# Performance work log

Hardware: AMD Instinct MI355X
Metric: run time of the kernel (lower is better)

## Reference

```python
import jax, jax.numpy as jnp
import numpy as np

NBINS = (128, 64, 32)
N_REGIONS = 5000
N_REGIONS_OI = 500
N_POINTS = 262144
SUM_H = sum(NBINS)            # 224
SUM_W = sum(n - 1 for n in NBINS)  # 221


def _spline_level(x, uw_region, uh_pt, local_ix):
    """One quadratic-spline level.
    x: [N] inputs in [0,1); uw_region: [R, n-1] region unnormalized widths;
    uh_pt: [N, n] per-point unnormalized heights (embedding + delta);
    local_ix: [N] int mapping points -> rows of uw_region.
    """
    # region-level widths / bin locations (calculate_widths / calculate_bin_locations)
    widths = jax.nn.softmax(uw_region, axis=-1)                # [R, n-1]
    bl = jnp.cumsum(widths, axis=-1)
    bl = bl.at[:, -1].set(1.0)
    bin_locations = jnp.pad(bl, ((0, 0), (1, 0)))              # [R, n]

    # gather per point (index_select(0, local_region_ix))
    widths_pt = widths[local_ix]                               # [N, n-1]
    bin_loc_pt = bin_locations[local_ix]                       # [N, n]

    # calculate_heights: exp then normalize so trapezoid integral == 1
    he = jnp.exp(uh_pt)                                        # [N, n]
    area = jnp.sum(0.5 * (he[:, :-1] + he[:, 1:]) * widths_pt, axis=-1, keepdims=True)
    heights = he / area                                        # [N, n]

    # calculate_bin_left_cdf
    cdf = jnp.cumsum(0.5 * (heights[:, :-1] + heights[:, 1:]) * widths_pt, axis=-1)
    cdf = cdf.at[:, -1].set(1.0)
    bin_left_cdf = jnp.pad(cdf, ((0, 0), (1, 0)))              # [N, n]

    # searchsorted(bin_locations, x, side='left') - 1, clamped to valid bins
    n = bin_loc_pt.shape[-1]
    bin_idx = jnp.clip(jnp.sum(bin_loc_pt < x[:, None], axis=-1) - 1, 0, n - 2)  # [N]

    take = lambda a, i: jnp.take_along_axis(a, i[:, None], axis=-1)[:, 0]
    in_loc = take(bin_loc_pt, bin_idx)
    in_w = take(widths_pt, bin_idx)
    in_cdf = take(bin_left_cdf, bin_idx)
    h_l = take(heights, bin_idx)
    h_r = take(heights, bin_idx + 1)

    alpha = (x - in_loc) / in_w
    a = 0.5 * (h_r - h_l) * in_w
    b = h_l * in_w
    out = a * alpha * alpha + b * alpha + in_cdf
    logabsdet = jnp.log(alpha * (h_r - h_l) + h_l)
    return out, logabsdet


def setup_inputs() -> dict:
    key = jax.random.key(0)
    k1, k2, k3, k4, k5, k6 = jax.random.split(key, 6)
    x = jax.random.uniform(k1, (N_POINTS,), dtype=jnp.float32)
    regions_oi = jax.random.randint(k2, (N_REGIONS_OI,), 0, N_REGIONS, dtype=jnp.int32)
    local_region_ix = jax.random.randint(k3, (N_POINTS,), 0, N_REGIONS_OI, dtype=jnp.int32)
    delta = jax.random.normal(k4, (N_POINTS, SUM_H), dtype=jnp.float32)
    # learned sparse embedding tables (init to random for a nontrivial baseline)
    heights_emb = 0.1 * jax.random.normal(k5, (N_REGIONS, SUM_H), dtype=jnp.float32)
    widths_emb = 0.1 * jax.random.normal(k6, (N_REGIONS, SUM_W), dtype=jnp.float32)
    return {"x": x, "regions_oi": regions_oi, "local_region_ix": local_region_ix,
            "delta": delta, "heights_emb": heights_emb, "widths_emb": widths_emb}


def reference(x, regions_oi, local_region_ix, delta, heights_emb, widths_emb):
    uh_all = heights_emb[regions_oi]   # [R, 224]
    uw_all = widths_emb[regions_oi]    # [R, 221]
    out = x
    logdet = jnp.zeros_like(x)
    oh = 0
    ow = 0
    for n in NBINS:
        uw = uw_all[:, ow:ow + (n - 1)]                               # [R, n-1]
        uh_pt = uh_all[local_region_ix][:, oh:oh + n] + delta[:, oh:oh + n]  # [N, n]
        out, ld = _spline_level(out, uw, uh_pt, local_region_ix)
        logdet = logdet + ld
        oh += n
        ow += n - 1
    return out, logdet
```

## Files before the change

### kernel.cpp

```cpp
#include <hip/hip_runtime.h>

#define NPOINTS 262144
#define SUMH 224
#define SUMW 221
#define NREG 500

__device__ __forceinline__ float rlane(float v, int l) {
  return __int_as_float(__builtin_amdgcn_readlane(__float_as_int(v), l));
}
template<int CTRL>
__device__ __forceinline__ float dpp0(float x) {
  return __int_as_float(__builtin_amdgcn_update_dpp(0, __float_as_int(x), CTRL, 0xF, 0xF, true));
}
template<int CTRL, int RM>
__device__ __forceinline__ float dpp_rm(float x) {
  return __int_as_float(__builtin_amdgcn_update_dpp(0, __float_as_int(x), CTRL, RM, 0xF, false));
}
template<int CTRL>
__device__ __forceinline__ float dpp_max_(float x) {
  return fmaxf(x, __int_as_float(__builtin_amdgcn_update_dpp(__float_as_int(x), __float_as_int(x), CTRL, 0xF, 0xF, false)));
}
__device__ __forceinline__ float wave_sum(float x) {
  x += dpp0<0x111>(x); x += dpp0<0x112>(x); x += dpp0<0x114>(x); x += dpp0<0x118>(x);
  x += dpp_rm<0x142, 0xA>(x); x += dpp_rm<0x143, 0xC>(x);
  return rlane(x, 63);
}
__device__ __forceinline__ float wave_max(float x) {
  x = dpp_max_<0x111>(x); x = dpp_max_<0x112>(x); x = dpp_max_<0x114>(x);
  x = dpp_max_<0x118>(x); x = dpp_max_<0x142>(x); x = dpp_max_<0x143>(x);
  return rlane(x, 63);
}
__device__ __forceinline__ float wave_scan_incl(float x) {
  x += dpp0<0x111>(x); x += dpp0<0x112>(x); x += dpp0<0x114>(x); x += dpp0<0x118>(x);
  x += dpp_rm<0x142, 0xA>(x);
  x += dpp_rm<0x143, 0xC>(x);
  return x;
}
__device__ __forceinline__ float grp_sum(float x) {
  x += dpp0<0xB1>(x);
  x += dpp0<0x4E>(x);
  x += dpp0<0x141>(x);
  x += dpp0<0x140>(x);
  return x;
}


template<int M, int SRC, int DST, int NB>
__device__ __forceinline__ void region_level(const float* __restrict__ wrow,
    float* __restrict__ BL, float* __restrict__ HW, float* __restrict__ HS,
    int lane, float* lds)
{
  float v0 = (lane < M) ? wrow[SRC + lane] : -1e30f;
  float v1 = -1e30f;
  if constexpr (NB == 128) { if (lane + 64 < M) v1 = wrow[SRC + lane + 64]; }
  float m = wave_max(fmaxf(v0, v1));
  float e0 = __expf(v0 - m);
  float e1 = (NB == 128) ? __expf(v1 - m) : 0.0f;
  float s = wave_sum(e0 + e1);
  float inv = 1.0f / s;
  if (lane < NB) lds[lane] = e0;
  if constexpr (NB == 128) lds[lane + 64] = e1;
  __syncthreads();
  if (lane < NB) {
    HW[DST + lane] = 0.5f * e0 * inv;
    float prev = (lane == 0) ? 0.0f : lds[lane - 1];
    HS[DST + lane] = 0.5f * (e0 + prev) * inv;
  }
  if constexpr (NB == 128) {
    HW[DST + lane + 64] = 0.5f * e1 * inv;
    HS[DST + lane + 64] = 0.5f * (e1 + lds[lane + 63]) * inv;
  }
  float incl0 = wave_scan_incl(e0);
  if (lane == 0) BL[DST] = 0.0f;
  if (lane < M) BL[DST + 1 + lane] = (lane == M - 1) ? 1.0f : incl0 * inv;
  if constexpr (NB == 128) {
    float incl1 = wave_scan_incl(e1) + rlane(incl0, 63);
    int k = 64 + lane;
    if (k < M) BL[DST + 1 + k] = (k == M - 1) ? 1.0f : incl1 * inv;
  }
  __syncthreads();
}

__global__ void __launch_bounds__(64) region_kernel(
    const int* __restrict__ roi, const float* __restrict__ wemb,
    float* __restrict__ wsBL, float* __restrict__ wsHW, float* __restrict__ wsHS)
{
  __shared__ float lds[128];
  int rix = blockIdx.x;
  int lane = threadIdx.x;
  int greg = roi[rix];
  const float* wrow = wemb + (size_t)greg * SUMW;
  float* BL = wsBL + (size_t)rix * SUMH;
  float* HW = wsHW + (size_t)rix * SUMH;
  float* HS = wsHS + (size_t)rix * SUMH;
  region_level<127,   0,   0, 128>(wrow, BL, HW, HS, lane, lds);
  region_level< 63, 127, 128,  64>(wrow, BL, HW, HS, lane, lds);
  region_level< 31, 190, 192,  32>(wrow, BL, HW, HS, lane, lds);
}


template<int NB, int OFF, int C>
struct Lv {
  float he[C], t[C], bl[C], hw[C];
  float larea, invarea;

  __device__ __forceinline__ void prep(const float* __restrict__ U,
      const float* __restrict__ D, const float* __restrict__ BLt,
      const float* __restrict__ HWt, const float* __restrict__ HSt, int s)
  {
    if constexpr (C >= 4) {
#pragma unroll
      for (int v = 0; v < C / 4; ++v) {
        int c0 = OFF + (s * (C / 4) + v) * 4;
        float4 a = *(const float4*)(U   + c0);
        float4 b = *(const float4*)(D   + c0);
        float4 e = *(const float4*)(BLt + c0);
        float4 f = *(const float4*)(HWt + c0);
        float4 g = *(const float4*)(HSt + c0);
        he[4*v+0] = __expf(a.x + b.x); he[4*v+1] = __expf(a.y + b.y);
        he[4*v+2] = __expf(a.z + b.z); he[4*v+3] = __expf(a.w + b.w);
        t[4*v+0] = he[4*v+0] * g.x; t[4*v+1] = he[4*v+1] * g.y;
        t[4*v+2] = he[4*v+2] * g.z; t[4*v+3] = he[4*v+3] * g.w;
        bl[4*v+0]=e.x; bl[4*v+1]=e.y; bl[4*v+2]=e.z; bl[4*v+3]=e.w;
        hw[4*v+0]=f.x; hw[4*v+1]=f.y; hw[4*v+2]=f.z; hw[4*v+3]=f.w;
      }
    } else {
      int c0 = OFF + s * 2;
      float2 a = *(const float2*)(U   + c0);
      float2 b = *(const float2*)(D   + c0);
      float2 e = *(const float2*)(BLt + c0);
      float2 f = *(const float2*)(HWt + c0);
      float2 g = *(const float2*)(HSt + c0);
      he[0] = __expf(a.x + b.x); he[1] = __expf(a.y + b.y);
      t[0] = he[0] * g.x; t[1] = he[1] * g.y;
      bl[0]=e.x; bl[1]=e.y; hw[0]=f.x; hw[1]=f.y;
    }
    float asum = 0.0f;
#pragma unroll
    for (int i = 0; i < C; ++i) asum += t[i];
    float area = grp_sum(asum);
    larea = __log2f(area);
    invarea = __builtin_amdgcn_rcpf(area);
  }

  __device__ __forceinline__ void apply(float& xv, float& logdet, int s) {
    float f[C];
#pragma unroll
    for (int i = 0; i < C; ++i) f[i] = (bl[i] < xv) ? 1.0f : 0.0f;
    if (s == 0)  f[0]     = 1.0f;
    if (s == 15) f[C - 1] = 0.0f;
    float fN  = dpp0<0x101>(f[0]);
    float heN = dpp0<0x101>(he[0]);
    float hl = 0.0f, hr = 0.0f, loc = 0.0f, hwm = 0.0f, pt = 0.0f;
#pragma unroll
    for (int i = 0; i < C; ++i) {
      float fnext  = (i < C - 1) ? f[i + 1]  : fN;
      float henext = (i < C - 1) ? he[i + 1] : heN;
      float mi = f[i] * (1.0f - fnext);
      hl  += he[i] * mi;
      hr  += henext * mi;
      loc += bl[i] * mi;
      hwm += hw[i] * mi;
      pt  += t[i] * f[i];
    }
    hl  = grp_sum(hl);
    hr  = grp_sum(hr);
    loc = grp_sum(loc);
    hwm = grp_sum(hwm);
    pt  = grp_sum(pt);
    float part = pt - hl * hwm;
    float inw = 2.0f * hwm;
    float alpha = (xv - loc) * __builtin_amdgcn_rcpf(inw);
    float dh = hr - hl;
    xv = ((0.5f * dh * alpha + hl) * alpha * inw + part) * invarea;
    logdet += (__log2f(alpha * dh + hl) - larea) * 0.69314718055994531f;
  }
};

__global__ void __launch_bounds__(256) spline_kernel(
    const float* __restrict__ x, const int* __restrict__ roi,
    const int* __restrict__ lix, const float* __restrict__ delta,
    const float* __restrict__ hemb,
    const float* __restrict__ wsBL, const float* __restrict__ wsHW,
    const float* __restrict__ wsHS, float* __restrict__ out)
{
  int tid  = (int)(blockIdx.x * blockDim.x + threadIdx.x);
  int wid  = tid >> 6;
  int lane = (int)(threadIdx.x & 63);
  int grp  = lane >> 4;
  int s    = lane & 15;
  int pid  = wid * 4 + grp;

  float xv = x[pid];
  int r    = lix[pid];
  int greg = roi[r];
  const float* U   = hemb  + (size_t)greg * SUMH;
  const float* D   = delta + (size_t)pid  * SUMH;
  const float* BLt = wsBL  + (size_t)r    * SUMH;
  const float* HWt = wsHW  + (size_t)r    * SUMH;
  const float* HSt = wsHS  + (size_t)r    * SUMH;

  Lv<128,   0, 8> L0;
  Lv< 64, 128, 4> L1;
  Lv< 32, 192, 2> L2;
  float logdet = 0.0f;
  L0.prep(U, D, BLt, HWt, HSt, s);
  L1.prep(U, D, BLt, HWt, HSt, s);
  L0.apply(xv, logdet, s);
  L2.prep(U, D, BLt, HWt, HSt, s);
  L1.apply(xv, logdet, s);
  L2.apply(xv, logdet, s);

  if (s == 0) {
    out[pid] = xv;
    out[NPOINTS + pid] = logdet;
  }
}


extern "C" void kernel_launch(void* const* d_in, const int* in_sizes, int n_in,
                              void* d_out, int out_size, void* d_ws, size_t ws_size,
                              hipStream_t stream) {
  const float* x     = (const float*)d_in[0];
  const int*   roi   = (const int*)  d_in[1];
  const int*   lix   = (const int*)  d_in[2];
  const float* delta = (const float*)d_in[3];
  const float* hemb  = (const float*)d_in[4];
  const float* wemb  = (const float*)d_in[5];

  float* wsBL = (float*)d_ws;
  float* wsHW = wsBL + (size_t)NREG * SUMH;
  float* wsHS = wsHW + (size_t)NREG * SUMH;

  region_kernel<<<NREG, 64, 0, stream>>>(roi, wemb, wsBL, wsHW, wsHS);
  spline_kernel<<<NPOINTS / 16, 256, 0, stream>>>(x, roi, lix, delta, hemb,
                                                  wsBL, wsHW, wsHS, (float*)d_out);
}
```

Before: 358.7 us.

## Map each point to 32 lanes instead of 16 in spline kernel

Each point is now processed by a half-wave of 32 lanes rather than 16, so each lane holds fewer bins per level (4/2/1 instead of 8/4/2). Group reductions gain a ds_swizzle step, and the neighbour exchange moves from DPP row shift to ds_bpermute. The grid doubles and launch bounds now request 8 blocks per CU. The aim is to cut per-lane registers and raise occupancy to hide the memory latency of the delta stream, at the cost of more cross-lane LDS-path operations and more redundant per-point scalar work.

```diff
diff --git a/kernel.cpp b/kernel.cpp
--- a/kernel.cpp
+++ b/kernel.cpp
@@ -36,12 +36,16 @@
   x += dpp_rm<0x143, 0xC>(x);
   return x;
 }
-__device__ __forceinline__ float grp_sum(float x) {
+__device__ __forceinline__ float grp32_sum(float x) {
   x += dpp0<0xB1>(x);
   x += dpp0<0x4E>(x);
   x += dpp0<0x141>(x);
   x += dpp0<0x140>(x);
+  x += __int_as_float(__builtin_amdgcn_ds_swizzle(__float_as_int(x), 0x401F));
   return x;
+}
+__device__ __forceinline__ float bperm(int byteidx, float v) {
+  return __int_as_float(__builtin_amdgcn_ds_bpermute(byteidx, __float_as_int(v)));
 }
 
 
@@ -99,85 +103,88 @@
 }
 
 
-template<int NB, int OFF, int C>
-struct Lv {
-  float he[C], t[C], bl[C], hw[C];
-  float larea, invarea;
-
-  __device__ __forceinline__ void prep(const float* __restrict__ U,
-      const float* __restrict__ D, const float* __restrict__ BLt,
-      const float* __restrict__ HWt, const float* __restrict__ HSt, int s)
-  {
-    if constexpr (C >= 4) {
+template<int OFF, int C>
+__device__ __forceinline__ void prep(const float* __restrict__ U,
+    const float* __restrict__ D, const float* __restrict__ BLt,
+    const float* __restrict__ HWt, const float* __restrict__ HSt, int s,
+    float (&he)[C], float (&t)[C], float (&bl)[C], float (&hw)[C],
+    float& larea, float& invarea)
+{
+  if constexpr (C == 4) {
+    int c0 = OFF + s * 4;
+    float4 a = *(const float4*)(U   + c0);
+    float4 b = *(const float4*)(D   + c0);
+    float4 e = *(const float4*)(BLt + c0);
+    float4 f = *(const float4*)(HWt + c0);
+    float4 g = *(const float4*)(HSt + c0);
+    he[0] = __expf(a.x + b.x); he[1] = __expf(a.y + b.y);
+    he[2] = __expf(a.z + b.z); he[3] = __expf(a.w + b.w);
+    t[0] = he[0] * g.x; t[1] = he[1] * g.y; t[2] = he[2] * g.z; t[3] = he[3] * g.w;
+    bl[0] = e.x; bl[1] = e.y; bl[2] = e.z; bl[3] = e.w;
+    hw[0] = f.x; hw[1] = f.y; hw[2] = f.z; hw[3] = f.w;
+  } else if constexpr (C == 2) {
+    int c0 = OFF + s * 2;
+    float2 a = *(const float2*)(U   + c0);
+    float2 b = *(const float2*)(D   + c0);
+    float2 e = *(const float2*)(BLt + c0);
+    float2 f = *(const float2*)(HWt + c0);
+    float2 g = *(const float2*)(HSt + c0);
+    he[0] = __expf(a.x + b.x); he[1] = __expf(a.y + b.y);
+    t[0] = he[0] * g.x; t[1] = he[1] * g.y;
+    bl[0] = e.x; bl[1] = e.y; hw[0] = f.x; hw[1] = f.y;
+  } else {
+    int c0 = OFF + s;
+    he[0] = __expf(U[c0] + D[c0]);
+    t[0]  = he[0] * HSt[c0];
+    bl[0] = BLt[c0];
+    hw[0] = HWt[c0];
+  }
+  float a_ = 0.0f;
 #pragma unroll
-      for (int v = 0; v < C / 4; ++v) {
-        int c0 = OFF + (s * (C / 4) + v) * 4;
-        float4 a = *(const float4*)(U   + c0);
-        float4 b = *(const float4*)(D   + c0);
-        float4 e = *(const float4*)(BLt + c0);
-        float4 f = *(const float4*)(HWt + c0);
-        float4 g = *(const float4*)(HSt + c0);
-        he[4*v+0] = __expf(a.x + b.x); he[4*v+1] = __expf(a.y + b.y);
-        he[4*v+2] = __expf(a.z + b.z); he[4*v+3] = __expf(a.w + b.w);
-        t[4*v+0] = he[4*v+0] * g.x; t[4*v+1] = he[4*v+1] * g.y;
-        t[4*v+2] = he[4*v+2] * g.z; t[4*v+3] = he[4*v+3] * g.w;
-        bl[4*v+0]=e.x; bl[4*v+1]=e.y; bl[4*v+2]=e.z; bl[4*v+3]=e.w;
-        hw[4*v+0]=f.x; hw[4*v+1]=f.y; hw[4*v+2]=f.z; hw[4*v+3]=f.w;
-      }
-    } else {
-      int c0 = OFF + s * 2;
-      float2 a = *(const float2*)(U   + c0);
-      float2 b = *(const float2*)(D   + c0);
-      float2 e = *(const float2*)(BLt + c0);
-      float2 f = *(const float2*)(HWt + c0);
-      float2 g = *(const float2*)(HSt + c0);
-      he[0] = __expf(a.x + b.x); he[1] = __expf(a.y + b.y);
-      t[0] = he[0] * g.x; t[1] = he[1] * g.y;
-      bl[0]=e.x; bl[1]=e.y; hw[0]=f.x; hw[1]=f.y;
-    }
-    float asum = 0.0f;
+  for (int i = 0; i < C; ++i) a_ += t[i];
+  float area = grp32_sum(a_);
+  larea = __log2f(area);
+  invarea = __builtin_amdgcn_rcpf(area);
+}
+
+template<int C>
+__device__ __forceinline__ void apply(float& xv, float& logdet, int s, int nb_idx,
+    const float (&he)[C], const float (&t)[C], const float (&bl)[C],
+    const float (&hw)[C], float larea, float invarea)
+{
+  float f[C];
 #pragma unroll
-    for (int i = 0; i < C; ++i) asum += t[i];
-    float area = grp_sum(asum);
-    larea = __log2f(area);
-    invarea = __builtin_amdgcn_rcpf(area);
-  }
-
-  __device__ __forceinline__ void apply(float& xv, float& logdet, int s) {
-    float f[C];
+  for (int i = 0; i < C; ++i) f[i] = (bl[i] < xv) ? 1.0f : 0.0f;
+  if (s == 0)  f[0]     = 1.0f;
+  if (s == 31) f[C - 1] = 0.0f;
+  float fN  = bperm(nb_idx, f[0]);
+  float heN = bperm(nb_idx, he[0]);
+  float hl = 0.0f, hr = 0.0f, loc = 0.0f, hwm = 0.0f, pt = 0.0f;
 #pragma unroll
-    for (int i = 0; i < C; ++i) f[i] = (bl[i] < xv) ? 1.0f : 0.0f;
-    if (s == 0)  f[0]     = 1.0f;
-    if (s == 15) f[C - 1] = 0.0f;
-    float fN  = dpp0<0x101>(f[0]);
-    float heN = dpp0<0x101>(he[0]);
-    float hl = 0.0f, hr = 0.0f, loc = 0.0f, hwm = 0.0f, pt = 0.0f;
-#pragma unroll
-    for (int i = 0; i < C; ++i) {
-      float fnext  = (i < C - 1) ? f[i + 1]  : fN;
-      float henext = (i < C - 1) ? he[i + 1] : heN;
-      float mi = f[i] * (1.0f - fnext);
-      hl  += he[i] * mi;
-      hr  += henext * mi;
-      loc += bl[i] * mi;
-      hwm += hw[i] * mi;
-      pt  += t[i] * f[i];
-    }
-    hl  = grp_sum(hl);
-    hr  = grp_sum(hr);
-    loc = grp_sum(loc);
-    hwm = grp_sum(hwm);
-    pt  = grp_sum(pt);
-    float part = pt - hl * hwm;
-    float inw = 2.0f * hwm;
-    float alpha = (xv - loc) * __builtin_amdgcn_rcpf(inw);
-    float dh = hr - hl;
-    xv = ((0.5f * dh * alpha + hl) * alpha * inw + part) * invarea;
-    logdet += (__log2f(alpha * dh + hl) - larea) * 0.69314718055994531f;
-  }
-};
-
-__global__ void __launch_bounds__(256) spline_kernel(
+  for (int i = 0; i < C; ++i) {
+    float fnext  = (i < C - 1) ? f[i + 1]  : fN;
+    float henext = (i < C - 1) ? he[i + 1] : heN;
+    float mi = f[i] * (1.0f - fnext);
+    hl  += he[i] * mi;
+    hr  += henext * mi;
+    loc += bl[i] * mi;
+    hwm += hw[i] * mi;
+    pt  += t[i] * f[i];
+  }
+  hl  = grp32_sum(hl);
+  hr  = grp32_sum(hr);
+  loc = grp32_sum(loc);
+  hwm = grp32_sum(hwm);
+  pt  = grp32_sum(pt);
+  float part = pt - hl * hwm;
+  float inw = 2.0f * hwm;
+  float alpha = (xv - loc) * __builtin_amdgcn_rcpf(inw);
+  float dh = hr - hl;
+  xv = ((0.5f * dh * alpha + hl) * alpha * inw + part) * invarea;
+  logdet += (__log2f(alpha * dh + hl) - larea) * 0.69314718055994531f;
+}
+
+__global__ void __launch_bounds__(256, 8) spline_kernel(
     const float* __restrict__ x, const int* __restrict__ roi,
     const int* __restrict__ lix, const float* __restrict__ delta,
     const float* __restrict__ hemb,
@@ -187,9 +194,10 @@
   int tid  = (int)(blockIdx.x * blockDim.x + threadIdx.x);
   int wid  = tid >> 6;
   int lane = (int)(threadIdx.x & 63);
-  int grp  = lane >> 4;
-  int s    = lane & 15;
-  int pid  = wid * 4 + grp;
+  int grp  = lane >> 5;
+  int s    = lane & 31;
+  int pid  = wid * 2 + grp;
+  int nb_idx = ((lane + 1) & 63) << 2;
 
   float xv = x[pid];
   int r    = lix[pid];
@@ -200,16 +208,17 @@
   const float* HWt = wsHW  + (size_t)r    * SUMH;
   const float* HSt = wsHS  + (size_t)r    * SUMH;
 
-  Lv<128,   0, 8> L0;
-  Lv< 64, 128, 4> L1;
-  Lv< 32, 192, 2> L2;
+  float he0[4], t0[4], bl0[4], hw0[4], la0, ia0;
+  float he1[2], t1[2], bl1[2], hw1[2], la1, ia1;
+  float he2[1], t2[1], bl2[1], hw2[1], la2, ia2;
+  prep<  0, 4>(U, D, BLt, HWt, HSt, s, he0, t0, bl0, hw0, la0, ia0);
+  prep<128, 2>(U, D, BLt, HWt, HSt, s, he1, t1, bl1, hw1, la1, ia1);
+  prep<192, 1>(U, D, BLt, HWt, HSt, s, he2, t2, bl2, hw2, la2, ia2);
+
   float logdet = 0.0f;
-  L0.prep(U, D, BLt, HWt, HSt, s);
-  L1.prep(U, D, BLt, HWt, HSt, s);
-  L0.apply(xv, logdet, s);
-  L2.prep(U, D, BLt, HWt, HSt, s);
-  L1.apply(xv, logdet, s);
-  L2.apply(xv, logdet, s);
+  apply<4>(xv, logdet, s, nb_idx, he0, t0, bl0, hw0, la0, ia0);
+  apply<2>(xv, logdet, s, nb_idx, he1, t1, bl1, hw1, la1, ia1);
+  apply<1>(xv, logdet, s, nb_idx, he2, t2, bl2, hw2, la2, ia2);
 
   if (s == 0) {
     out[pid] = xv;
@@ -233,6 +242,6 @@
   float* wsHS = wsHW + (size_t)NREG * SUMH;
 
   region_kernel<<<NREG, 64, 0, stream>>>(roi, wemb, wsBL, wsHW, wsHS);
-  spline_kernel<<<NPOINTS / 16, 256, 0, stream>>>(x, roi, lix, delta, hemb,
-                                                  wsBL, wsHW, wsHS, (float*)d_out);
-}
+  spline_kernel<<<NPOINTS / 8, 256, 0, stream>>>(x, roi, lix, delta, hemb,
+                                                 wsBL, wsHW, wsHS, (float*)d_out);
+}
```

After: 361.3 us. About the same (+0.7%).

## Sort points by region and process per-region blocks reusing region tables

Applied to the files above, without the earlier changes.

Adds histogram, scan and scatter kernels that bucket point indices by local region. The spline kernel now launches blocks per (region, chunk). Each block loads the region's embedding, bin-location, half-width and half-sum rows into registers once, then loops over 64 sorted points, streaming only each point's delta row. This cuts the per-point re-gathering of four 224-float region rows, at the cost of extra launches, atomics and a fixed cap of 16 chunks × 64 = 1024 points per region; points beyond that cap would be silently dropped.

```diff
diff --git a/kernel.cpp b/kernel.cpp
--- a/kernel.cpp
+++ b/kernel.cpp
@@ -4,6 +4,7 @@
 #define SUMH 224
 #define SUMW 221
 #define NREG 500
+#define CPB 16
 
 __device__ __forceinline__ float rlane(float v, int l) {
   return __int_as_float(__builtin_amdgcn_readlane(__float_as_int(v), l));
@@ -44,7 +45,6 @@
   return x;
 }
 
-
 template<int M, int SRC, int DST, int NB>
 __device__ __forceinline__ void region_level(const float* __restrict__ wrow,
     float* __restrict__ BL, float* __restrict__ HW, float* __restrict__ HS,
@@ -56,8 +56,8 @@
   float m = wave_max(fmaxf(v0, v1));
   float e0 = __expf(v0 - m);
   float e1 = (NB == 128) ? __expf(v1 - m) : 0.0f;
-  float s = wave_sum(e0 + e1);
-  float inv = 1.0f / s;
+  float sm = wave_sum(e0 + e1);
+  float inv = 1.0f / sm;
   if (lane < NB) lds[lane] = e0;
   if constexpr (NB == 128) lds[lane + 64] = e1;
   __syncthreads();
@@ -98,122 +98,182 @@
   region_level< 31, 190, 192,  32>(wrow, BL, HW, HS, lane, lds);
 }
 
-
-template<int NB, int OFF, int C>
-struct Lv {
-  float he[C], t[C], bl[C], hw[C];
-  float larea, invarea;
-
-  __device__ __forceinline__ void prep(const float* __restrict__ U,
-      const float* __restrict__ D, const float* __restrict__ BLt,
-      const float* __restrict__ HWt, const float* __restrict__ HSt, int s)
-  {
-    if constexpr (C >= 4) {
-#pragma unroll
-      for (int v = 0; v < C / 4; ++v) {
-        int c0 = OFF + (s * (C / 4) + v) * 4;
-        float4 a = *(const float4*)(U   + c0);
-        float4 b = *(const float4*)(D   + c0);
-        float4 e = *(const float4*)(BLt + c0);
-        float4 f = *(const float4*)(HWt + c0);
-        float4 g = *(const float4*)(HSt + c0);
-        he[4*v+0] = __expf(a.x + b.x); he[4*v+1] = __expf(a.y + b.y);
-        he[4*v+2] = __expf(a.z + b.z); he[4*v+3] = __expf(a.w + b.w);
-        t[4*v+0] = he[4*v+0] * g.x; t[4*v+1] = he[4*v+1] * g.y;
-        t[4*v+2] = he[4*v+2] * g.z; t[4*v+3] = he[4*v+3] * g.w;
-        bl[4*v+0]=e.x; bl[4*v+1]=e.y; bl[4*v+2]=e.z; bl[4*v+3]=e.w;
-        hw[4*v+0]=f.x; hw[4*v+1]=f.y; hw[4*v+2]=f.z; hw[4*v+3]=f.w;
-      }
-    } else {
-      int c0 = OFF + s * 2;
-      float2 a = *(const float2*)(U   + c0);
-      float2 b = *(const float2*)(D   + c0);
-      float2 e = *(const float2*)(BLt + c0);
-      float2 f = *(const float2*)(HWt + c0);
-      float2 g = *(const float2*)(HSt + c0);
-      he[0] = __expf(a.x + b.x); he[1] = __expf(a.y + b.y);
-      t[0] = he[0] * g.x; t[1] = he[1] * g.y;
-      bl[0]=e.x; bl[1]=e.y; hw[0]=f.x; hw[1]=f.y;
-    }
-    float asum = 0.0f;
-#pragma unroll
-    for (int i = 0; i < C; ++i) asum += t[i];
-    float area = grp_sum(asum);
-    larea = __log2f(area);
-    invarea = __builtin_amdgcn_rcpf(area);
-  }
-
-  __device__ __forceinline__ void apply(float& xv, float& logdet, int s) {
-    float f[C];
-#pragma unroll
-    for (int i = 0; i < C; ++i) f[i] = (bl[i] < xv) ? 1.0f : 0.0f;
-    if (s == 0)  f[0]     = 1.0f;
-    if (s == 15) f[C - 1] = 0.0f;
-    float fN  = dpp0<0x101>(f[0]);
-    float heN = dpp0<0x101>(he[0]);
-    float hl = 0.0f, hr = 0.0f, loc = 0.0f, hwm = 0.0f, pt = 0.0f;
-#pragma unroll
-    for (int i = 0; i < C; ++i) {
-      float fnext  = (i < C - 1) ? f[i + 1]  : fN;
-      float henext = (i < C - 1) ? he[i + 1] : heN;
-      float mi = f[i] * (1.0f - fnext);
-      hl  += he[i] * mi;
-      hr  += henext * mi;
-      loc += bl[i] * mi;
-      hwm += hw[i] * mi;
-      pt  += t[i] * f[i];
-    }
-    hl  = grp_sum(hl);
-    hr  = grp_sum(hr);
-    loc = grp_sum(loc);
-    hwm = grp_sum(hwm);
-    pt  = grp_sum(pt);
-    float part = pt - hl * hwm;
-    float inw = 2.0f * hwm;
-    float alpha = (xv - loc) * __builtin_amdgcn_rcpf(inw);
-    float dh = hr - hl;
-    xv = ((0.5f * dh * alpha + hl) * alpha * inw + part) * invarea;
-    logdet += (__log2f(alpha * dh + hl) - larea) * 0.69314718055994531f;
-  }
-};
-
-__global__ void __launch_bounds__(256) spline_kernel(
+__global__ void __launch_bounds__(512) zero_kernel(int* __restrict__ hist) {
+  hist[threadIdx.x] = 0;
+}
+
+__global__ void __launch_bounds__(256) hist_kernel(
+    const int* __restrict__ lix, int* __restrict__ hist)
+{
+  __shared__ int h[512];
+  for (int i = threadIdx.x; i < 512; i += 256) h[i] = 0;
+  __syncthreads();
+  int base = blockIdx.x * 4096;
+#pragma unroll
+  for (int k = 0; k < 16; ++k) {
+    int p = base + k * 256 + threadIdx.x;
+    atomicAdd(&h[lix[p]], 1);
+  }
+  __syncthreads();
+  for (int i = threadIdx.x; i < 500; i += 256) {
+    int v = h[i];
+    if (v) atomicAdd(&hist[i], v);
+  }
+}
+
+__global__ void __launch_bounds__(512) scan_kernel(
+    const int* __restrict__ hist, int* __restrict__ offs, int* __restrict__ cursor)
+{
+  __shared__ int sb[512];
+  int t = threadIdx.x;
+  int v = (t < NREG) ? hist[t] : 0;
+  sb[t] = v;
+  __syncthreads();
+  for (int d = 1; d < 512; d <<= 1) {
+    int add = (t >= d) ? sb[t - d] : 0;
+    __syncthreads();
+    sb[t] += add;
+    __syncthreads();
+  }
+  if (t < NREG) {
+    int excl = sb[t] - v;
+    offs[t] = excl;
+    cursor[t] = excl;
+  }
+}
+
+__global__ void __launch_bounds__(256) scatter_kernel(
+    const int* __restrict__ lix, int* __restrict__ cursor, int* __restrict__ sorted)
+{
+  int p = blockIdx.x * 256 + threadIdx.x;
+  int r = lix[p];
+  int slot = atomicAdd(&cursor[r], 1);
+  sorted[slot] = p;
+}
+
+
+template<int C>
+__device__ __forceinline__ void apply16(float& xv, float& logdet, int s,
+    const float (&u)[C], const float (&d)[C], const float (&bl)[C],
+    const float (&hw)[C], const float (&hs)[C])
+{
+  float he[C], t[C], f[C];
+#pragma unroll
+  for (int i = 0; i < C; ++i) { he[i] = __expf(u[i] + d[i]); t[i] = he[i] * hs[i]; }
+#pragma unroll
+  for (int i = 0; i < C; ++i) f[i] = (bl[i] < xv) ? 1.0f : 0.0f;
+  if (s == 0)  f[0]     = 1.0f;
+  if (s == 15) f[C - 1] = 0.0f;
+  float fN  = dpp0<0x101>(f[0]);
+  float heN = dpp0<0x101>(he[0]);
+  float area = 0.0f, hl = 0.0f, hr = 0.0f, loc = 0.0f, hwm = 0.0f, pt = 0.0f;
+#pragma unroll
+  for (int i = 0; i < C; ++i) {
+    float fnext  = (i < C - 1) ? f[i + 1]  : fN;
+    float henext = (i < C - 1) ? he[i + 1] : heN;
+    float mi = f[i] * (1.0f - fnext);
+    area += t[i];
+    hl  += he[i] * mi;
+    hr  += henext * mi;
+    loc += bl[i] * mi;
+    hwm += hw[i] * mi;
+    pt  += t[i] * f[i];
+  }
+  area = grp_sum(area);
+  hl  = grp_sum(hl);
+  hr  = grp_sum(hr);
+  loc = grp_sum(loc);
+  hwm = grp_sum(hwm);
+  pt  = grp_sum(pt);
+  float larea = __log2f(area);
+  float invarea = __builtin_amdgcn_rcpf(area);
+  float part = pt - hl * hwm;
+  float inw = 2.0f * hwm;
+  float alpha = (xv - loc) * __builtin_amdgcn_rcpf(inw);
+  float dh = hr - hl;
+  xv = ((0.5f * dh * alpha + hl) * alpha * inw + part) * invarea;
+  logdet += (__log2f(alpha * dh + hl) - larea) * 0.69314718055994531f;
+}
+
+__device__ __forceinline__ void ld8(float (&a)[8], const float* p) {
+  float4 q0 = *(const float4*)(p);
+  float4 q1 = *(const float4*)(p + 4);
+  a[0]=q0.x; a[1]=q0.y; a[2]=q0.z; a[3]=q0.w;
+  a[4]=q1.x; a[5]=q1.y; a[6]=q1.z; a[7]=q1.w;
+}
+__device__ __forceinline__ void ld4(float (&a)[4], const float* p) {
+  float4 q = *(const float4*)(p);
+  a[0]=q.x; a[1]=q.y; a[2]=q.z; a[3]=q.w;
+}
+__device__ __forceinline__ void ld2(float (&a)[2], const float* p) {
+  float2 q = *(const float2*)(p);
+  a[0]=q.x; a[1]=q.y;
+}
+
+__global__ void __launch_bounds__(256, 4) spline_kernel(
     const float* __restrict__ x, const int* __restrict__ roi,
-    const int* __restrict__ lix, const float* __restrict__ delta,
-    const float* __restrict__ hemb,
+    const float* __restrict__ delta, const float* __restrict__ hemb,
     const float* __restrict__ wsBL, const float* __restrict__ wsHW,
-    const float* __restrict__ wsHS, float* __restrict__ out)
-{
-  int tid  = (int)(blockIdx.x * blockDim.x + threadIdx.x);
-  int wid  = tid >> 6;
+    const float* __restrict__ wsHS, const int* __restrict__ hist,
+    const int* __restrict__ offs, const int* __restrict__ sorted,
+    float* __restrict__ out)
+{
+  int region = blockIdx.x / CPB;
+  int chunk  = blockIdx.x % CPB;
+  int cnt = hist[region];
+  if (chunk * 64 >= cnt) return;
+  int base  = offs[region] + chunk * 64;
+  int lastv = offs[region] + cnt - 1;
+
   int lane = (int)(threadIdx.x & 63);
+  int wv   = (int)(threadIdx.x >> 6);
   int grp  = lane >> 4;
   int s    = lane & 15;
-  int pid  = wid * 4 + grp;
-
-  float xv = x[pid];
-  int r    = lix[pid];
-  int greg = roi[r];
-  const float* U   = hemb  + (size_t)greg * SUMH;
-  const float* D   = delta + (size_t)pid  * SUMH;
-  const float* BLt = wsBL  + (size_t)r    * SUMH;
-  const float* HWt = wsHW  + (size_t)r    * SUMH;
-  const float* HSt = wsHS  + (size_t)r    * SUMH;
-
-  Lv<128,   0, 8> L0;
-  Lv< 64, 128, 4> L1;
-  Lv< 32, 192, 2> L2;
-  float logdet = 0.0f;
-  L0.prep(U, D, BLt, HWt, HSt, s);
-  L1.prep(U, D, BLt, HWt, HSt, s);
-  L0.apply(xv, logdet, s);
-  L2.prep(U, D, BLt, HWt, HSt, s);
-  L1.apply(xv, logdet, s);
-  L2.apply(xv, logdet, s);
-
-  if (s == 0) {
-    out[pid] = xv;
-    out[NPOINTS + pid] = logdet;
+
+  int greg = roi[region];
+  const float* Ur  = hemb + (size_t)greg  * SUMH;
+  const float* BLr = wsBL + (size_t)region * SUMH;
+  const float* HWr = wsHW + (size_t)region * SUMH;
+  const float* HSr = wsHS + (size_t)region * SUMH;
+
+  float u0[8], bl0[8], hw0[8], hs0[8];
+  float u1[4], bl1[4], hw1[4], hs1[4];
+  float u2[2], bl2[2], hw2[2], hs2[2];
+  ld8(u0, Ur + 8 * s);         ld8(bl0, BLr + 8 * s);
+  ld8(hw0, HWr + 8 * s);       ld8(hs0, HSr + 8 * s);
+  ld4(u1, Ur + 128 + 4 * s);   ld4(bl1, BLr + 128 + 4 * s);
+  ld4(hw1, HWr + 128 + 4 * s); ld4(hs1, HSr + 128 + 4 * s);
+  ld2(u2, Ur + 192 + 2 * s);   ld2(bl2, BLr + 192 + 2 * s);
+  ld2(hw2, HWr + 192 + 2 * s); ld2(hs2, HSr + 192 + 2 * s);
+
+  int idx = base + wv * 4 + grp;
+  int idxc = min(idx, lastv);
+  int pid = sorted[idxc];
+
+#pragma unroll
+  for (int it = 0; it < 4; ++it) {
+    bool valid = idx <= lastv;
+    float xv = x[pid];
+    const float* D = delta + (size_t)pid * SUMH;
+    float d0[8], d1[4], d2[2];
+    ld8(d0, D + 8 * s);
+    ld4(d1, D + 128 + 4 * s);
+    ld2(d2, D + 192 + 2 * s);
+
+    int nidx = idx + 16;
+    int pid_n = sorted[min(nidx, lastv)];
+
+    float logdet = 0.0f;
+    apply16<8>(xv, logdet, s, u0, d0, bl0, hw0, hs0);
+    apply16<4>(xv, logdet, s, u1, d1, bl1, hw1, hs1);
+    apply16<2>(xv, logdet, s, u2, d2, bl2, hw2, hs2);
+
+    if (valid && s == 0) {
+      out[pid] = xv;
+      out[NPOINTS + pid] = logdet;
+    }
+    idx = nidx;
+    pid = pid_n;
   }
 }
 
@@ -231,8 +291,17 @@
   float* wsBL = (float*)d_ws;
   float* wsHW = wsBL + (size_t)NREG * SUMH;
   float* wsHS = wsHW + (size_t)NREG * SUMH;
-
+  int*   hist   = (int*)(wsHS + (size_t)NREG * SUMH);
+  int*   offs   = hist + 512;
+  int*   cursor = offs + 512;
+  int*   sorted = cursor + 512;
+
+  zero_kernel<<<1, 512, 0, stream>>>(hist);
+  hist_kernel<<<NPOINTS / 4096, 256, 0, stream>>>(lix, hist);
   region_kernel<<<NREG, 64, 0, stream>>>(roi, wemb, wsBL, wsHW, wsHS);
-  spline_kernel<<<NPOINTS / 16, 256, 0, stream>>>(x, roi, lix, delta, hemb,
-                                                  wsBL, wsHW, wsHS, (float*)d_out);
-}
+  scan_kernel<<<1, 512, 0, stream>>>(hist, offs, cursor);
+  scatter_kernel<<<NPOINTS / 256, 256, 0, stream>>>(lix, cursor, sorted);
+  spline_kernel<<<NREG * CPB, 256, 0, stream>>>(x, roi, delta, hemb,
+                                                wsBL, wsHW, wsHS,
+                                                hist, offs, sorted, (float*)d_out);
+}
```

Result: slower. 461.9 us (+28.8%).
